# Performance work log

Hardware: AMD Instinct MI355X
Metric: run time of the kernel (lower is better)

Reference implementation:

```python
import jax, jax.numpy as jnp
import numpy as np

N_CLASSES = 256
PER_CLASS = 128
N_SUPPORT = 5
N_QUERY = PER_CLASS - N_SUPPORT  # 123
N_VIEW = 2
D = 384
N = N_CLASSES * PER_CLASS  # 32768


def setup_inputs() -> dict:
    key = jax.random.key(0)
    k1, k2 = jax.random.split(key, 2)
    reps = jax.random.normal(k1, (N, N_VIEW, D), dtype=jnp.float32)
    # block-sorted labels: class c occupies rows [c*PER_CLASS, (c+1)*PER_CLASS)
    labels = (jnp.arange(N, dtype=jnp.int32) // PER_CLASS).astype(jnp.int32)
    return {"reps": reps, "labels": labels}


def reference(reps, labels):
    # labels are block-sorted per class, so the original's
    # labels.eq(c).nonzero()[:n_support] / [n_support:] gathers are static reshapes.
    reps_r = reps.reshape(N_CLASSES, PER_CLASS, N_VIEW, D)
    # class-mean prototypes over the support set: [C, V, D]
    prototypes = reps_r[:, :N_SUPPORT].mean(axis=1)
    # query samples: [C*N_QUERY, V, D]
    queries = reps_r[:, N_SUPPORT:].reshape(N_CLASSES * N_QUERY, N_VIEW, D)

    x2 = jnp.sum(queries * queries, axis=-1)            # [n, V]
    y2 = jnp.sum(prototypes * prototypes, axis=-1)      # [m, V]
    xy = jnp.einsum('nvd,mvd->nmv', queries, prototypes)  # [n, m, V]
    dists = x2[:, None, :] + y2[None, :, :] - 2.0 * xy

    # log_softmax over the prototype (class) axis
    log_p_y = jax.nn.log_softmax(-dists, axis=1)
    log_p_y = log_p_y.reshape(N_CLASSES, N_QUERY, N_CLASSES, N_VIEW)

    # gather the true-class log-prob for each query / view
    cls = jnp.arange(N_CLASSES)
    correct = log_p_y[cls, :, cls, :]  # [C, N_QUERY, V]
    loss = -correct.mean()
    return loss
```

## Files before the change

### kernel.cpp

```cpp
#include <hip/hip_runtime.h>
#include <hip/hip_bf16.h>
#include <math.h>

#define NCLS 256
#define PER_CLASS 128
#define NSUP 5
#define NQRY 123
#define NVIEW 2
#define DD 384
#define NQ_TOT (NCLS * NQRY)
#define BM 128
#define BK 32
#define NKT (DD / BK)
#define PS 32

typedef __attribute__((ext_vector_type(8))) short short8;
typedef __attribute__((ext_vector_type(4))) float floatx4;

union FragU { uint4 u; short8 s; };
union PkU { __hip_bfloat162 b2; unsigned int u; };

__device__ __forceinline__ unsigned int cvt2bf(float lo, float hi) {
    PkU p;
    p.b2 = __float22bfloat162_rn(make_float2(lo, hi));
    return p.u;
}

__device__ __forceinline__ void gll16(const ushort* g, ushort* l) {
    __builtin_amdgcn_global_load_lds(
        (const __attribute__((address_space(1))) unsigned int*)g,
        (__attribute__((address_space(3))) unsigned int*)l, 16, 0, 0);
}

#define BARRIER() asm volatile("s_waitcnt lgkmcnt(0)\n\ts_barrier" ::: "memory")
#define WAITVM(n) asm volatile("s_waitcnt vmcnt(" #n ")" ::: "memory")

__global__ __launch_bounds__(384) void proto_kernel(const float* __restrict__ reps,
                                                    ushort* __restrict__ pbf,
                                                    float* __restrict__ y2,
                                                    float* __restrict__ out) {
    __shared__ float wp[6];
    const int b = blockIdx.x;
    const int c = b & 255, v = b >> 8;
    const int d = threadIdx.x;
    if (b == 0 && d == 0) out[0] = 0.f;
    const float* p = reps + ((size_t)(c * PER_CLASS) * NVIEW + v) * DD + d;
    float s = 0.f;
#pragma unroll
    for (int k = 0; k < NSUP; ++k) s += p[(size_t)k * NVIEW * DD];
    s *= 0.2f;
    __hip_bfloat16 h = __float2bfloat16(s);
    pbf[(size_t)b * DD + d] = *reinterpret_cast<ushort*>(&h);
    float q = s * s;
#pragma unroll
    for (int o = 1; o < 64; o <<= 1) q += __shfl_xor(q, o);
    if ((d & 63) == 0) wp[d >> 6] = q;
    __syncthreads();
    if (d == 0) y2[b] = wp[0] + wp[1] + wp[2] + wp[3] + wp[4] + wp[5];
}

__global__ __launch_bounds__(512, 2) void main_kernel(const float* __restrict__ reps,
                                                      const ushort* __restrict__ pbf,
                                                      const float* __restrict__ y2g,
                                                      float* __restrict__ out) {
    __shared__ ushort q_lds[NKT * BM * 32];
    __shared__ ushort p_lds[2][NCLS * PS];

    const int t = threadIdx.x;
    const int v = blockIdx.y;
    const int q0 = blockIdx.x * BM;
    const int wave = t >> 6;
    const int lane = t & 63;
    const int col = lane & 15;
    const int quad = lane >> 4;
    const int wm = wave >> 2;
    const int wn = wave & 3;

    const ushort* psrc = pbf + (size_t)(v * NCLS + wave * 32 + (lane >> 2)) * DD
                             + (((lane & 3) ^ ((lane >> 3) & 3)) << 3);

    const int sP = (col >> 1) & 3;
    const int pbase = (wn * 64 + col) * PS + ((quad ^ sP) << 3);

#define GLLP(kt, b)                                                                \
    do {                                                                           \
        gll16(psrc + (kt) * BK, &p_lds[b][wave * 1024]);                           \
        gll16(psrc + 16 * DD + (kt) * BK, &p_lds[b][wave * 1024 + 512]);           \
    } while (0)

    GLLP(0, 0);
    GLLP(1, 1);

    {
        const int qrow = t >> 2;
        const int qp = t & 3;
        const int nq = q0 + qrow;
        const float* qsrc = reps +
            (size_t)((nq / NQRY) * PER_CLASS + NSUP + (nq % NQRY)) * (NVIEW * DD) +
            v * DD + qp * 96;
        const int swzq = (qrow >> 1) & 3;

        float4 A[24];
#pragma unroll
        for (int i = 0; i < 24; ++i) A[i] = *(const float4*)(qsrc + i * 4);
#pragma unroll
        for (int g = 0; g < 3; ++g) {
            const int kt = qp * 3 + g;
#pragma unroll
            for (int q = 0; q < 4; ++q) {
                uint4 w;
                w.x = cvt2bf(A[g * 8 + 2 * q].x, A[g * 8 + 2 * q].y);
                w.y = cvt2bf(A[g * 8 + 2 * q].z, A[g * 8 + 2 * q].w);
                w.z = cvt2bf(A[g * 8 + 2 * q + 1].x, A[g * 8 + 2 * q + 1].y);
                w.w = cvt2bf(A[g * 8 + 2 * q + 1].z, A[g * 8 + 2 * q + 1].w);
                *(uint4*)&q_lds[kt * 4096 + qrow * 32 + ((q ^ swzq) << 3)] = w;
            }
        }
    }

    floatx4 acc[4][4];
#pragma unroll
    for (int mt = 0; mt < 4; ++mt)
#pragma unroll
        for (int nt = 0; nt < 4; ++nt) acc[mt][nt] = (floatx4)0.f;

#define COMPUTE(kt, pb)                                                            \
    do {                                                                           \
        short8 af[4];                                                              \
        _Pragma("unroll") for (int mt = 0; mt < 4; ++mt) {                         \
            FragU f;                                                               \
            f.u = *(const uint4*)&q_lds[(kt) * 4096 +                              \
                (wm * 64 + mt * 16 + col) * 32 + ((quad ^ sP) << 3)];              \
            af[mt] = f.s;                                                          \
        }                                                                          \
        _Pragma("unroll") for (int nt = 0; nt < 4; ++nt) {                         \
            FragU bb;                                                              \
            bb.u = *(const uint4*)&p_lds[pb][pbase + nt * 16 * PS];                \
            _Pragma("unroll") for (int mt = 0; mt < 4; ++mt)                       \
                acc[mt][nt] = __builtin_amdgcn_mfma_f32_16x16x32_bf16(af[mt], bb.s, acc[mt][nt], 0, 0, 0); \
        }                                                                          \
    } while (0)

    WAITVM(0);
    BARRIER();

#pragma unroll
    for (int kt = 0; kt < NKT; ++kt) {
        COMPUTE(kt, kt & 1);
        if (kt == NKT - 1) break;
        BARRIER();
        if (kt + 2 < NKT) {
            GLLP(kt + 2, kt & 1);
            WAITVM(2);
        } else {
            WAITVM(0);
        }
        BARRIER();
    }

    __syncthreads();
    float* eplds = (float*)&p_lds[0][0];
    float (*pmx)[4] = (float(*)[4])eplds;
    float (*pse)[4] = (float(*)[4])(eplds + 512);
    float* wred = eplds + 1024;

    float y2c[4];
#pragma unroll
    for (int nt = 0; nt < 4; ++nt) y2c[nt] = y2g[v * NCLS + wn * 64 + nt * 16 + col];

    float corr = 0.f;
#pragma unroll
    for (int mt = 0; mt < 4; ++mt) {
#pragma unroll
        for (int r = 0; r < 4; ++r) {
            const int qloc = wm * 64 + mt * 16 + quad * 4 + r;
            const int n = q0 + qloc;
            const int cn = n / NQRY;
            float s[4];
            float mx = -1e30f;
#pragma unroll
            for (int nt = 0; nt < 4; ++nt) {
                s[nt] = 2.f * acc[mt][nt][r] - y2c[nt];
                mx = fmaxf(mx, s[nt]);
                if (cn == wn * 64 + nt * 16 + col) corr += s[nt];
            }
#pragma unroll
            for (int o = 1; o < 16; o <<= 1) mx = fmaxf(mx, __shfl_xor(mx, o));
            float e = 0.f;
#pragma unroll
            for (int nt = 0; nt < 4; ++nt) e += __expf(s[nt] - mx);
#pragma unroll
            for (int o = 1; o < 16; o <<= 1) e += __shfl_xor(e, o);
            if (col == 0) { pmx[qloc][wn] = mx; pse[qloc][wn] = e; }
        }
    }
#pragma unroll
    for (int o = 1; o < 64; o <<= 1) corr += __shfl_xor(corr, o);
    if (lane == 0) wred[wave] = corr;
    __syncthreads();

    float lval = 0.f;
    if (t < BM) {
        float m0 = pmx[t][0], m1 = pmx[t][1], m2 = pmx[t][2], m3 = pmx[t][3];
        float M = fmaxf(fmaxf(m0, m1), fmaxf(m2, m3));
        float E = pse[t][0] * __expf(m0 - M) + pse[t][1] * __expf(m1 - M) +
                  pse[t][2] * __expf(m2 - M) + pse[t][3] * __expf(m3 - M);
        lval = M + __logf(E);
    }
#pragma unroll
    for (int o = 1; o < 64; o <<= 1) lval += __shfl_xor(lval, o);
    if (lane == 0) wred[8 + wave] = lval;
    __syncthreads();

    if (t == 0) {
        float tot = (wred[8] + wred[9] + wred[10] + wred[11] +
                     wred[12] + wred[13] + wred[14] + wred[15]) -
                    (wred[0] + wred[1] + wred[2] + wred[3] +
                     wred[4] + wred[5] + wred[6] + wred[7]);
        atomicAdd(out, tot * (1.f / (float)(NQ_TOT * NVIEW)));
    }
}

extern "C" void kernel_launch(void* const* d_in, const int* in_sizes, int n_in,
                              void* d_out, int out_size, void* d_ws, size_t ws_size,
                              hipStream_t stream) {
    const float* reps = (const float*)d_in[0];
    float* ws = (float*)d_ws;
    ushort* pbf = (ushort*)ws;
    float* y2 = (float*)(pbf + NVIEW * NCLS * DD);
    float* out = (float*)d_out;

    proto_kernel<<<dim3(NVIEW * NCLS), dim3(DD), 0, stream>>>(reps, pbf, y2, out);
    main_kernel<<<dim3(NQ_TOT / BM, NVIEW), dim3(512), 0, stream>>>(reps, pbf, y2, out);
}
```

Before: 177.8 us.

## Halve query tile to 64 rows for two blocks per CU and reorder loads

Shrinks the query tile from 128 to 64 rows, which cuts the query LDS slab roughly in half so two blocks can share a CU, and raises launch bounds to match. Each thread now loads 12 float4 segments instead of 24, and the prototype global-to-LDS prefetch is issued after the query loads. The initial wait is relaxed to vmcnt(2), and a kt-dependent XOR swizzle is added to the query LDS layout. The goal is more latency hiding for the memory-bound query stream, at the cost of twice as many blocks each re-reading the full prototype tiles from L2.

```diff
diff --git a/kernel.cpp b/kernel.cpp
--- a/kernel.cpp
+++ b/kernel.cpp
@@ -9,10 +9,11 @@
 #define NVIEW 2
 #define DD 384
 #define NQ_TOT (NCLS * NQRY)
-#define BM 128
+#define BM 64
 #define BK 32
 #define NKT (DD / BK)
 #define PS 32
+#define QSLAB 2048
 
 typedef __attribute__((ext_vector_type(8))) short short8;
 typedef __attribute__((ext_vector_type(4))) float floatx4;
@@ -59,11 +60,11 @@
     if (d == 0) y2[b] = wp[0] + wp[1] + wp[2] + wp[3] + wp[4] + wp[5];
 }
 
-__global__ __launch_bounds__(512, 2) void main_kernel(const float* __restrict__ reps,
+__global__ __launch_bounds__(512, 4) void main_kernel(const float* __restrict__ reps,
                                                       const ushort* __restrict__ pbf,
                                                       const float* __restrict__ y2g,
                                                       float* __restrict__ out) {
-    __shared__ ushort q_lds[NKT * BM * 32];
+    __shared__ ushort q_lds[NKT * QSLAB];
     __shared__ ushort p_lds[2][NCLS * PS];
 
     const int t = threadIdx.x;
@@ -88,60 +89,60 @@
         gll16(psrc + 16 * DD + (kt) * BK, &p_lds[b][wave * 1024 + 512]);           \
     } while (0)
 
-    GLLP(0, 0);
-    GLLP(1, 1);
-
     {
-        const int qrow = t >> 2;
-        const int qp = t & 3;
+        const int qrow = t >> 3;
+        const int seg = t & 7;
         const int nq = q0 + qrow;
         const float* qsrc = reps +
             (size_t)((nq / NQRY) * PER_CLASS + NSUP + (nq % NQRY)) * (NVIEW * DD) +
-            v * DD + qp * 96;
-        const int swzq = (qrow >> 1) & 3;
-
-        float4 A[24];
-#pragma unroll
-        for (int i = 0; i < 24; ++i) A[i] = *(const float4*)(qsrc + i * 4);
-#pragma unroll
-        for (int g = 0; g < 3; ++g) {
-            const int kt = qp * 3 + g;
-#pragma unroll
-            for (int q = 0; q < 4; ++q) {
-                uint4 w;
-                w.x = cvt2bf(A[g * 8 + 2 * q].x, A[g * 8 + 2 * q].y);
-                w.y = cvt2bf(A[g * 8 + 2 * q].z, A[g * 8 + 2 * q].w);
-                w.z = cvt2bf(A[g * 8 + 2 * q + 1].x, A[g * 8 + 2 * q + 1].y);
-                w.w = cvt2bf(A[g * 8 + 2 * q + 1].z, A[g * 8 + 2 * q + 1].w);
-                *(uint4*)&q_lds[kt * 4096 + qrow * 32 + ((q ^ swzq) << 3)] = w;
-            }
+            v * DD + seg * 48;
+
+        float4 A[12];
+#pragma unroll
+        for (int i = 0; i < 12; ++i) A[i] = *(const float4*)(qsrc + i * 4);
+
+        GLLP(0, 0);
+        GLLP(1, 1);
+
+        const int swzr = (qrow >> 1) & 3;
+#pragma unroll
+        for (int i = 0; i < 6; ++i) {
+            const int kk = seg * 48 + i * 8;
+            const int kt = kk >> 5;
+            const int c = (kk & 31) >> 3;
+            uint4 w;
+            w.x = cvt2bf(A[2 * i].x, A[2 * i].y);
+            w.y = cvt2bf(A[2 * i].z, A[2 * i].w);
+            w.z = cvt2bf(A[2 * i + 1].x, A[2 * i + 1].y);
+            w.w = cvt2bf(A[2 * i + 1].z, A[2 * i + 1].w);
+            *(uint4*)&q_lds[kt * QSLAB + qrow * 32 + ((c ^ swzr ^ (kt & 3)) << 3)] = w;
         }
     }
 
-    floatx4 acc[4][4];
-#pragma unroll
-    for (int mt = 0; mt < 4; ++mt)
+    floatx4 acc[2][4];
+#pragma unroll
+    for (int mt = 0; mt < 2; ++mt)
 #pragma unroll
         for (int nt = 0; nt < 4; ++nt) acc[mt][nt] = (floatx4)0.f;
 
 #define COMPUTE(kt, pb)                                                            \
     do {                                                                           \
-        short8 af[4];                                                              \
-        _Pragma("unroll") for (int mt = 0; mt < 4; ++mt) {                         \
+        short8 af[2];                                                              \
+        _Pragma("unroll") for (int mt = 0; mt < 2; ++mt) {                         \
             FragU f;                                                               \
-            f.u = *(const uint4*)&q_lds[(kt) * 4096 +                              \
-                (wm * 64 + mt * 16 + col) * 32 + ((quad ^ sP) << 3)];              \
+            f.u = *(const uint4*)&q_lds[(kt) * QSLAB +                             \
+                (wm * 32 + mt * 16 + col) * 32 + ((quad ^ sP ^ ((kt) & 3)) << 3)]; \
             af[mt] = f.s;                                                          \
         }                                                                          \
         _Pragma("unroll") for (int nt = 0; nt < 4; ++nt) {                         \
             FragU bb;                                                              \
             bb.u = *(const uint4*)&p_lds[pb][pbase + nt * 16 * PS];                \
-            _Pragma("unroll") for (int mt = 0; mt < 4; ++mt)                       \
+            _Pragma("unroll") for (int mt = 0; mt < 2; ++mt)                       \
                 acc[mt][nt] = __builtin_amdgcn_mfma_f32_16x16x32_bf16(af[mt], bb.s, acc[mt][nt], 0, 0, 0); \
         }                                                                          \
     } while (0)
 
-    WAITVM(0);
+    WAITVM(2);
     BARRIER();
 
 #pragma unroll
@@ -161,8 +162,8 @@
     __syncthreads();
     float* eplds = (float*)&p_lds[0][0];
     float (*pmx)[4] = (float(*)[4])eplds;
-    float (*pse)[4] = (float(*)[4])(eplds + 512);
-    float* wred = eplds + 1024;
+    float (*pse)[4] = (float(*)[4])(eplds + 256);
+    float* wred = eplds + 512;
 
     float y2c[4];
 #pragma unroll
@@ -170,10 +171,10 @@
 
     float corr = 0.f;
 #pragma unroll
-    for (int mt = 0; mt < 4; ++mt) {
+    for (int mt = 0; mt < 2; ++mt) {
 #pragma unroll
         for (int r = 0; r < 4; ++r) {
-            const int qloc = wm * 64 + mt * 16 + quad * 4 + r;
+            const int qloc = wm * 32 + mt * 16 + quad * 4 + r;
             const int n = q0 + qloc;
             const int cn = n / NQRY;
             float s[4];
```

Result: no change. 175.4 us (-1.3%).
